# Kernel tuning notes

Hardware: AMD Instinct MI355X
Metric: run time of the kernel (lower is better)

Reference implementation:

```python
import jax, jax.numpy as jnp
import numpy as np


def setup_inputs() -> dict:
    key = jax.random.key(0)
    k1, k2 = jax.random.split(key)
    B, S, HOP, L = 32, 524288, 256, 100
    frames = S // HOP
    # input hook asserts 0 <= phase <= 0.5
    wrapped_phase = jax.random.uniform(k1, (B, S), dtype=jnp.float32) * 0.5
    tables = jax.random.normal(k2, (B, frames + 1, L), dtype=jnp.float32)
    return {"wrapped_phase": wrapped_phase, "tables": tables, "hop_length": HOP}


def reference(wrapped_phase, tables, hop_length):
    # wrapped_phase: (B, S), hop_length divides S; tables: (B, S//hop + 1, L)
    B, S = wrapped_phase.shape
    frames = S // hop_length
    L = tables.shape[2]

    wp = wrapped_phase.reshape(B, frames, hop_length)          # (B, F, H)
    idx_raw = wp * L
    floor_idx = jnp.clip(idx_raw.astype(jnp.int32), 0, L - 1)  # (B, F, H)
    p = idx_raw - floor_idx.astype(wp.dtype)                   # frac along table axis

    # wrap-around pad of one sample along table axis: (B, F+1, L+1)
    padded = jnp.concatenate([tables, tables[:, :, :1]], axis=2)
    floor_flow = padded[:, :-1]                                # (B, F, L+1) frame t
    ceil_flow = padded[:, 1:]                                  # (B, F, L+1) frame t+1

    def lerp_table(flow):
        lo = jnp.take_along_axis(flow, floor_idx, axis=2)
        hi = jnp.take_along_axis(flow, floor_idx + 1, axis=2)
        return lo * (1 - p) + hi * p

    sel_floor = lerp_table(floor_flow)                         # (B, F, H)
    sel_ceil = lerp_table(ceil_flow)

    # interpolate across hop (frame) dimension
    p2 = jnp.arange(hop_length, dtype=wp.dtype) / hop_length   # (H,)
    final = sel_floor * (1 - p2) + sel_ceil * p2
    return final.reshape(B, -1)[:, :S]
```

## Files before the change

### kernel.cpp

```cpp
#include <hip/hip_runtime.h>

constexpr int HOP    = 256;
constexpr int L      = 100;
constexpr int FRAMES = 2048;
constexpr int B      = 32;
constexpr int FPB    = 4;

__global__ __launch_bounds__(256) void glottal_kernel(
    const float* __restrict__ wp,
    const float* __restrict__ tables,
    float* __restrict__ out)
{
    __shared__ float2 pairs[FPB][L + 1];

    const int tid = threadIdx.x;
    const int b   = blockIdx.x >> 9;
    const int g   = blockIdx.x & 511;
    const int f0  = g * FPB;

    const float* trow = tables + ((size_t)b * (FRAMES + 1) + (size_t)f0) * L;

    for (int i = tid; i < FPB * (L + 1); i += 256) {
        int r  = i / (L + 1);
        int c  = i - r * (L + 1);
        int cs = (c == L) ? 0 : c;
        pairs[r][c] = make_float2(trow[r * L + cs], trow[(r + 1) * L + cs]);
    }
    __syncthreads();

    const size_t base = ((size_t)b * FRAMES + (size_t)f0) * HOP + (size_t)tid * 4;
    float4 w = *reinterpret_cast<const float4*>(wp + base);

    const float2* row = pairs[tid >> 6];
    const int h0 = (tid & 63) * 4;

    float wv[4] = {w.x, w.y, w.z, w.w};
    float res[4];
#pragma unroll
    for (int j = 0; j < 4; ++j) {
        float idx_raw = wv[j] * (float)L;
        int fi = (int)idx_raw;
        fi = fi < 0 ? 0 : (fi > L - 1 ? L - 1 : fi);
        float p  = idx_raw - (float)fi;
        float2 lo = row[fi];
        float2 hi = row[fi + 1];
        float sf = lo.x + (hi.x - lo.x) * p;
        float sc = lo.y + (hi.y - lo.y) * p;
        float p2 = (float)(h0 + j) * (1.0f / HOP);
        res[j] = sf + (sc - sf) * p2;
    }

    *reinterpret_cast<float4*>(out + base) = make_float4(res[0], res[1], res[2], res[3]);
}

extern "C" void kernel_launch(void* const* d_in, const int* in_sizes, int n_in,
                              void* d_out, int out_size, void* d_ws, size_t ws_size,
                              hipStream_t stream) {
    const float* wp     = (const float*)d_in[0];
    const float* tables = (const float*)d_in[1];
    float* out = (float*)d_out;

    dim3 grid(B * (FRAMES / FPB));
    glottal_kernel<<<grid, 256, 0, stream>>>(wp, tables, out);
}
```

Before: 134.7 us.

## Process 8 frames per block with shared row table and nontemporal I/O

Doubles the frames per block to 8, so each thread handles 8 samples, and the grid is halved. The shared table changes from duplicated float2 pairs to a single set of FPB+1 rows, which cuts shared-memory staging and redundant table loads. Streaming loads and stores now use nontemporal builtins. In exchange there are fewer blocks in flight, and each sample needs four scalar LDS reads instead of two float2 reads.

```diff
diff --git a/kernel.cpp b/kernel.cpp
--- a/kernel.cpp
+++ b/kernel.cpp
@@ -4,53 +4,64 @@
 constexpr int L      = 100;
 constexpr int FRAMES = 2048;
 constexpr int B      = 32;
-constexpr int FPB    = 4;
+constexpr int FPB    = 8;
+constexpr int ROWS   = FPB + 1;
+constexpr int LSTR   = L + 1;
+
+typedef float f32x4 __attribute__((ext_vector_type(4)));
 
 __global__ __launch_bounds__(256) void glottal_kernel(
     const float* __restrict__ wp,
     const float* __restrict__ tables,
     float* __restrict__ out)
 {
-    __shared__ float2 pairs[FPB][L + 1];
+    __shared__ float tab[ROWS * LSTR];
 
     const int tid = threadIdx.x;
-    const int b   = blockIdx.x >> 9;
-    const int g   = blockIdx.x & 511;
+    const int b   = blockIdx.x >> 8;
+    const int g   = blockIdx.x & 255;
     const int f0  = g * FPB;
 
     const float* trow = tables + ((size_t)b * (FRAMES + 1) + (size_t)f0) * L;
 
-    for (int i = tid; i < FPB * (L + 1); i += 256) {
-        int r  = i / (L + 1);
-        int c  = i - r * (L + 1);
-        int cs = (c == L) ? 0 : c;
-        pairs[r][c] = make_float2(trow[r * L + cs], trow[(r + 1) * L + cs]);
+    for (int i = tid; i < ROWS * LSTR; i += 256) {
+        int r = i / LSTR;
+        int c = i - r * LSTR;
+        tab[i] = trow[r * L + (c == L ? 0 : c)];
     }
     __syncthreads();
 
-    const size_t base = ((size_t)b * FRAMES + (size_t)f0) * HOP + (size_t)tid * 4;
-    float4 w = *reinterpret_cast<const float4*>(wp + base);
+    const int r  = tid >> 5;
+    const int h0 = (tid & 31) * 8;
+    const float* __restrict__ row = tab + r * LSTR;
 
-    const float2* row = pairs[tid >> 6];
-    const int h0 = (tid & 63) * 4;
+    const size_t base = ((size_t)b * FRAMES + (size_t)f0) * HOP + (size_t)tid * 8;
 
-    float wv[4] = {w.x, w.y, w.z, w.w};
-    float res[4];
+    f32x4 w0 = __builtin_nontemporal_load(reinterpret_cast<const f32x4*>(wp + base));
+    f32x4 w1 = __builtin_nontemporal_load(reinterpret_cast<const f32x4*>(wp + base + 4));
+
+    float wv[8] = {w0.x, w0.y, w0.z, w0.w, w1.x, w1.y, w1.z, w1.w};
+    float res[8];
 #pragma unroll
-    for (int j = 0; j < 4; ++j) {
+    for (int j = 0; j < 8; ++j) {
         float idx_raw = wv[j] * (float)L;
         int fi = (int)idx_raw;
         fi = fi < 0 ? 0 : (fi > L - 1 ? L - 1 : fi);
         float p  = idx_raw - (float)fi;
-        float2 lo = row[fi];
-        float2 hi = row[fi + 1];
-        float sf = lo.x + (hi.x - lo.x) * p;
-        float sc = lo.y + (hi.y - lo.y) * p;
+        float a0 = row[fi];
+        float a1 = row[fi + 1];
+        float c0 = row[fi + LSTR];
+        float c1 = row[fi + LSTR + 1];
+        float sf = fmaf(a1 - a0, p, a0);
+        float sc = fmaf(c1 - c0, p, c0);
         float p2 = (float)(h0 + j) * (1.0f / HOP);
-        res[j] = sf + (sc - sf) * p2;
+        res[j] = fmaf(sc - sf, p2, sf);
     }
 
-    *reinterpret_cast<float4*>(out + base) = make_float4(res[0], res[1], res[2], res[3]);
+    f32x4 r0 = {res[0], res[1], res[2], res[3]};
+    f32x4 r1 = {res[4], res[5], res[6], res[7]};
+    __builtin_nontemporal_store(r0, reinterpret_cast<f32x4*>(out + base));
+    __builtin_nontemporal_store(r1, reinterpret_cast<f32x4*>(out + base + 4));
 }
 
 extern "C" void kernel_launch(void* const* d_in, const int* in_sizes, int n_in,
```

Result: slower. 137.6 us (+2.2%).
